# Kernel optimization log

Hardware: AMD Instinct MI355X
Metric: run time of the kernel (lower is better)

Reference implementation:

```python
import jax, jax.numpy as jnp
import numpy as np

MASK_GROUP = 8
RATIO = 0.125
K = max(1, min(MASK_GROUP, round(RATIO * MASK_GROUP)))  # = 1


def sparify_mask(outM):
    # top-k over the mask_group axis, scatter 1.0 at top-k positions
    _, idx = jax.lax.top_k(outM, K)              # [..., K]
    oh = jax.nn.one_hot(idx, outM.shape[-1], dtype=outM.dtype)  # [..., K, G]
    return jnp.sum(oh, axis=-2)                   # [..., G] 0/1 mask


def setup_inputs() -> dict:
    key = jax.random.key(0)
    ks = jax.random.split(key, 7)
    B, S, D, F = 4, 2048, 2048, 8192
    stdv = 1.0 / np.sqrt(F)
    u = lambda k, shape: jax.random.uniform(k, shape, jnp.float32, -stdv, stdv)
    return {
        "x": jax.random.normal(ks[0], (B, S, D), jnp.float32),
        "W1": u(ks[1], (F, D)),
        "b1": u(ks[2], (F,)),
        "Wm": u(ks[3], (MASK_GROUP, D)),
        "bm": u(ks[4], (MASK_GROUP,)),
        "W2": u(ks[5], (D, F)),
        "b2": u(ks[6], (D,)),
    }


def reference(x, W1, b1, Wm, bm, W2, b2):
    F_out = W1.shape[0]
    repeat_num = F_out // MASK_GROUP
    outL = jnp.einsum('bsd,fd->bsf', x, W1) + b1          # [B,S,F]
    outM = jax.nn.softmax(jnp.einsum('bsd,gd->bsg', x, Wm) + bm, axis=-1)  # [B,S,G]
    mask = sparify_mask(outM)                              # [B,S,G]
    gate = jnp.repeat(mask, repeat_num, axis=-1)           # [B,S,F]
    out2 = jax.nn.relu(outL * gate)
    out = jnp.einsum('bsf,df->bsd', out2, W2) + b2         # [B,S,D]
    return out
```

## Files before the change

### kernel.cpp

```cpp
#include <hip/hip_runtime.h>
#include <hip/hip_bf16.h>

#define T_TOK 8192
#define D_DIM 2048
#define F_DIM 8192
#define G_NUM 8
#define GF    1024

typedef __attribute__((ext_vector_type(8))) short bf16x8;
typedef __attribute__((ext_vector_type(4))) float f32x4;

__device__ __forceinline__ void async_load16(const void* g, void* l) {
    __builtin_amdgcn_global_load_lds(
        (const __attribute__((address_space(1))) unsigned int*)g,
        (__attribute__((address_space(3))) unsigned int*)l, 16, 0, 0);
}

__device__ __forceinline__ unsigned short f2bf(float f) {
    unsigned int u = __float_as_uint(f);
    unsigned int r = (u + 0x7fffu + ((u >> 16) & 1u)) >> 16;
    return (unsigned short)r;
}

__device__ __forceinline__ uint2 pack4(float4 v) {
    union { __hip_bfloat162 b; unsigned u; } c0, c1;
    c0.b = __float22bfloat162_rn({v.x, v.y});
    c1.b = __float22bfloat162_rn({v.z, v.w});
    uint2 r; r.x = c0.u; r.y = c1.u; return r;
}


__global__ void zero_cnt_kernel(int* __restrict__ cnt) {
    if (threadIdx.x < G_NUM) cnt[threadIdx.x] = 0;
}

__global__ __launch_bounds__(256)
void convert_kernel(const float* __restrict__ src, unsigned short* __restrict__ dst, int n) {
    int i = (blockIdx.x * 256 + threadIdx.x) * 8;
    if (i >= n) return;
    float4 a = *(const float4*)(src + i);
    float4 b = *(const float4*)(src + i + 4);
    uint2 p0 = pack4(a), p1 = pack4(b);
    uint4 o; o.x = p0.x; o.y = p0.y; o.z = p1.x; o.w = p1.y;
    *(uint4*)(dst + i) = o;
}

__global__ __launch_bounds__(256)
void gate_kernel(const float* __restrict__ x, const float* __restrict__ Wm,
                 const float* __restrict__ bm, int* __restrict__ cnt,
                 int* __restrict__ bucket) {
    const int wave  = threadIdx.x >> 6;
    const int lane  = threadIdx.x & 63;
    const int token = blockIdx.x * 4 + wave;
    const float* xr = x + (size_t)token * D_DIM;

    double acc[G_NUM];
#pragma unroll
    for (int g = 0; g < G_NUM; ++g) acc[g] = 0.0;

    for (int d = lane; d < D_DIM; d += 64) {
        float xv = xr[d];
#pragma unroll
        for (int g = 0; g < G_NUM; ++g)
            acc[g] += (double)xv * (double)Wm[g * D_DIM + d];
    }

#pragma unroll
    for (int g = 0; g < G_NUM; ++g) {
#pragma unroll
        for (int m = 32; m >= 1; m >>= 1)
            acc[g] += __shfl_xor(acc[g], m);
    }

    if (lane == 0) {
        double best = acc[0] + (double)bm[0];
        int bg = 0;
#pragma unroll
        for (int g = 1; g < G_NUM; ++g) {
            double v = acc[g] + (double)bm[g];
            if (v > best) { best = v; bg = g; }
        }
        int pos = atomicAdd(&cnt[bg], 1);
        bucket[bg * T_TOK + pos] = token;
    }
}

template <int KDIM, bool IS_G1, bool A_BF16, bool B_BF16>
__global__ __launch_bounds__(256)
void mfma_gemm(const void* __restrict__ Aop, const void* __restrict__ Bop,
               const float* __restrict__ bias,
               const int* __restrict__ cnt, const int* __restrict__ bucket,
               unsigned short* __restrict__ outH, float* __restrict__ outF) {
    const int g  = blockIdx.z;
    const int n  = cnt[g];
    const int t0 = blockIdx.y * 128;
    if (t0 >= n) return;
    const int nx0 = blockIdx.x * 128;
    const int tid  = threadIdx.x;
    const int lane = tid & 63;
    const int wv   = tid >> 6;

    __shared__ int toks[128];
    __shared__ __align__(16) unsigned short As[128 * 32];
    __shared__ __align__(16) unsigned short Bs[128 * 32];

    if (tid < 128) {
        int r = t0 + tid;
        if (r >= n) r = n - 1;
        toks[tid] = bucket[g * T_TOK + r];
    }
    __syncthreads();

    const size_t bstride = IS_G1 ? (size_t)KDIM : (size_t)F_DIM;
    const size_t brow0   = IS_G1 ? (size_t)(g * GF + nx0) : (size_t)nx0;
    const size_t bcol    = IS_G1 ? 0 : (size_t)(g * GF);

    const int lrow = tid >> 2;
    const int lseg = tid & 3;
    const unsigned short* aP0 = nullptr; const unsigned short* aP1 = nullptr;
    const unsigned short* bP0 = nullptr; const unsigned short* bP1 = nullptr;
    char *ldsA0 = nullptr, *ldsA1 = nullptr, *ldsB0 = nullptr, *ldsB1 = nullptr;
    if (A_BF16) {
        const unsigned short* Ab = (const unsigned short*)Aop;
        aP0 = Ab + (size_t)toks[lrow] * KDIM + lseg * 8;
        aP1 = Ab + (size_t)toks[64 + lrow] * KDIM + lseg * 8;
        ldsA0 = (char*)As + tid * 16;
        ldsA1 = (char*)As + 4096 + tid * 16;
    }
    if (B_BF16) {
        const unsigned short* Bb = (const unsigned short*)Bop;
        bP0 = Bb + (brow0 + lrow) * bstride + bcol + lseg * 8;
        bP1 = Bb + (brow0 + 64 + lrow) * bstride + bcol + lseg * 8;
        ldsB0 = (char*)Bs + tid * 16;
        ldsB1 = (char*)Bs + 4096 + tid * 16;
    }

    const int frw = tid >> 1;
    const int fsg = (tid & 1) * 16;
    const float* aF = nullptr; const float* bF = nullptr;
    char *ldsAf = nullptr, *ldsBf = nullptr;
    if (!A_BF16) {
        aF = (const float*)Aop + (size_t)toks[frw] * KDIM + fsg;
        ldsAf = (char*)As + frw * 64 + (tid & 1) * 32;
    }
    if (!B_BF16) {
        bF = (const float*)Bop + (brow0 + frw) * bstride + bcol + fsg;
        ldsBf = (char*)Bs + frw * 64 + (tid & 1) * 32;
    }

    f32x4 acc[4][4];
#pragma unroll
    for (int mi = 0; mi < 4; ++mi)
#pragma unroll
        for (int ni = 0; ni < 4; ++ni)
            acc[mi][ni] = (f32x4){0.f, 0.f, 0.f, 0.f};

    const int wr   = (wv >> 1) * 64;
    const int wc   = (wv & 1) * 64;
    const int frow = lane & 15;
    const int kh   = lane >> 4;

    for (int k0 = 0; k0 < KDIM; k0 += 32) {
        __syncthreads();
        if (A_BF16) { async_load16(aP0 + k0, ldsA0); async_load16(aP1 + k0, ldsA1); }
        if (B_BF16) { async_load16(bP0 + k0, ldsB0); async_load16(bP1 + k0, ldsB1); }
        if (!A_BF16) {
            float4 v0 = *(const float4*)(aF + k0);
            float4 v1 = *(const float4*)(aF + k0 + 4);
            float4 v2 = *(const float4*)(aF + k0 + 8);
            float4 v3 = *(const float4*)(aF + k0 + 12);
            uint2 p0 = pack4(v0), p1 = pack4(v1), p2 = pack4(v2), p3 = pack4(v3);
            uint4 w0; w0.x = p0.x; w0.y = p0.y; w0.z = p1.x; w0.w = p1.y;
            uint4 w1; w1.x = p2.x; w1.y = p2.y; w1.z = p3.x; w1.w = p3.y;
            *(uint4*)ldsAf = w0; *(uint4*)(ldsAf + 16) = w1;
        }
        if (!B_BF16) {
            float4 v0 = *(const float4*)(bF + k0);
            float4 v1 = *(const float4*)(bF + k0 + 4);
            float4 v2 = *(const float4*)(bF + k0 + 8);
            float4 v3 = *(const float4*)(bF + k0 + 12);
            uint2 p0 = pack4(v0), p1 = pack4(v1), p2 = pack4(v2), p3 = pack4(v3);
            uint4 w0; w0.x = p0.x; w0.y = p0.y; w0.z = p1.x; w0.w = p1.y;
            uint4 w1; w1.x = p2.x; w1.y = p2.y; w1.z = p3.x; w1.w = p3.y;
            *(uint4*)ldsBf = w0; *(uint4*)(ldsBf + 16) = w1;
        }
        __syncthreads();
        bf16x8 af[4], bfr[4];
#pragma unroll
        for (int mi = 0; mi < 4; ++mi)
            af[mi] = *(const bf16x8*)((const char*)As + (size_t)(wr + mi * 16 + frow) * 64 + kh * 16);
#pragma unroll
        for (int ni = 0; ni < 4; ++ni)
            bfr[ni] = *(const bf16x8*)((const char*)Bs + (size_t)(wc + ni * 16 + frow) * 64 + kh * 16);
#pragma unroll
        for (int mi = 0; mi < 4; ++mi)
#pragma unroll
            for (int ni = 0; ni < 4; ++ni)
                acc[mi][ni] = __builtin_amdgcn_mfma_f32_16x16x32_bf16(
                    af[mi], bfr[ni], acc[mi][ni], 0, 0, 0);
    }

    const float* bptr = bias + (IS_G1 ? (g * GF + nx0) : nx0);
    float bv[4];
#pragma unroll
    for (int ni = 0; ni < 4; ++ni) bv[ni] = bptr[wc + ni * 16 + frow];

#pragma unroll
    for (int mi = 0; mi < 4; ++mi) {
#pragma unroll
        for (int v = 0; v < 4; ++v) {
            int r = wr + mi * 16 + kh * 4 + v;
            if (t0 + r < n) {
                int tok = toks[r];
                if (IS_G1) {
                    unsigned short* dst = outH + (size_t)tok * GF + nx0 + wc + frow;
#pragma unroll
                    for (int ni = 0; ni < 4; ++ni) {
                        float o = fmaxf(acc[mi][ni][v] + bv[ni], 0.f);
                        dst[ni * 16] = f2bf(o);
                    }
                } else {
                    float* dst = outF + (size_t)tok * D_DIM + nx0 + wc + frow;
#pragma unroll
                    for (int ni = 0; ni < 4; ++ni)
                        dst[ni * 16] = acc[mi][ni][v] + bv[ni];
                }
            }
        }
    }
}

extern "C" void kernel_launch(void* const* d_in, const int* in_sizes, int n_in,
                              void* d_out, int out_size, void* d_ws, size_t ws_size,
                              hipStream_t stream) {
    const float* x  = (const float*)d_in[0];
    const float* W1 = (const float*)d_in[1];
    const float* b1 = (const float*)d_in[2];
    const float* Wm = (const float*)d_in[3];
    const float* bm = (const float*)d_in[4];
    const float* W2 = (const float*)d_in[5];
    const float* b2 = (const float*)d_in[6];
    float* out = (float*)d_out;

    int* cnt    = (int*)d_ws;
    int* bucket = (int*)((char*)d_ws + 1024);
    unsigned short* Hb  = (unsigned short*)((char*)d_ws + (1 << 19));
    unsigned short* xb  = Hb  + (size_t)T_TOK * GF;
    unsigned short* W1b = xb  + (size_t)T_TOK * D_DIM;
    unsigned short* W2b = W1b + (size_t)F_DIM * D_DIM;

    const bool fast = ws_size >= 117964800ull;
    const int NCVT = T_TOK * D_DIM;

    zero_cnt_kernel<<<1, 64, 0, stream>>>(cnt);
    gate_kernel<<<T_TOK / 4, 256, 0, stream>>>(x, Wm, bm, cnt, bucket);

    if (fast) {
        convert_kernel<<<NCVT / (256 * 8), 256, 0, stream>>>(x, xb, NCVT);
        convert_kernel<<<NCVT / (256 * 8), 256, 0, stream>>>(W1, W1b, NCVT);
        convert_kernel<<<NCVT / (256 * 8), 256, 0, stream>>>(W2, W2b, NCVT);
        mfma_gemm<D_DIM, true, true, true><<<dim3(GF / 128, T_TOK / 128, G_NUM), 256, 0, stream>>>(
            xb, W1b, b1, cnt, bucket, Hb, nullptr);
        mfma_gemm<GF, false, true, true><<<dim3(D_DIM / 128, T_TOK / 128, G_NUM), 256, 0, stream>>>(
            Hb, W2b, b2, cnt, bucket, nullptr, out);
    } else {
        mfma_gemm<D_DIM, true, false, false><<<dim3(GF / 128, T_TOK / 128, G_NUM), 256, 0, stream>>>(
            x, W1, b1, cnt, bucket, Hb, nullptr);
        mfma_gemm<GF, false, true, false><<<dim3(D_DIM / 128, T_TOK / 128, G_NUM), 256, 0, stream>>>(
            Hb, W2, b2, cnt, bucket, nullptr, out);
    }
}
```

Measured before the change: 468.2 us.

## Tile gate projection over token blocks and fuse x bf16 conversion into it

```diff
diff --git a/kernel.cpp b/kernel.cpp
--- a/kernel.cpp
+++ b/kernel.cpp
@@ -45,44 +45,99 @@
     *(uint4*)(dst + i) = o;
 }
 
+template <bool WRITE_XB>
+__global__ __launch_bounds__(64)
+void gate_partial_kernel(const float* __restrict__ x, const float* __restrict__ Wm,
+                         unsigned short* __restrict__ xb, double* __restrict__ part) {
+    const int q     = blockIdx.x;
+    const int t     = blockIdx.y;
+    const int lane  = threadIdx.x;
+    const int tok0  = t * 64;
+    const int kbase = q * 512;
+
+    __shared__ float wmS[8][512];
+    __shared__ float xs[64][68];
+
+    for (int i = lane * 4; i < 8 * 512; i += 64 * 4) {
+        int g = i >> 9, d = i & 511;
+        *(float4*)&wmS[g][d] = *(const float4*)(Wm + (size_t)g * D_DIM + kbase + d);
+    }
+
+    double acc[8] = {0, 0, 0, 0, 0, 0, 0, 0};
+
+    const int srow = lane >> 2;
+    const int scol = (lane & 3) * 4;
+
+    float4 v[16];
+#define LOAD_CHUNK(dbase_)                                                        \
+    _Pragma("unroll") for (int it = 0; it < 4; ++it)                              \
+    _Pragma("unroll") for (int ci = 0; ci < 4; ++ci) {                            \
+        int row = it * 16 + srow;                                                 \
+        int col = ci * 16 + scol;                                                 \
+        v[it * 4 + ci] = *(const float4*)(x + (size_t)(tok0 + row) * D_DIM +      \
+                                          kbase + (dbase_) + col);                \
+    }
+
+    LOAD_CHUNK(0)
+    __syncthreads();
+
+    for (int s = 0; s < 8; ++s) {
+        const int dbase = s * 64;
+#pragma unroll
+        for (int it = 0; it < 4; ++it)
+#pragma unroll
+            for (int ci = 0; ci < 4; ++ci) {
+                int row = it * 16 + srow;
+                int col = ci * 16 + scol;
+                *(float4*)&xs[row][col] = v[it * 4 + ci];
+                if (WRITE_XB) {
+                    uint2 p = pack4(v[it * 4 + ci]);
+                    *(uint2*)(xb + (size_t)(tok0 + row) * D_DIM + kbase + dbase + col) = p;
+                }
+            }
+        __syncthreads();
+        if (s < 7) { LOAD_CHUNK(dbase + 64) }
+#pragma unroll
+        for (int j4 = 0; j4 < 16; ++j4) {
+            float4 xv = *(const float4*)&xs[lane][j4 * 4];
+#pragma unroll
+            for (int g = 0; g < 8; ++g) {
+                float4 wv = *(const float4*)&wmS[g][dbase + j4 * 4];
+                acc[g] += (double)xv.x * (double)wv.x;
+                acc[g] += (double)xv.y * (double)wv.y;
+                acc[g] += (double)xv.z * (double)wv.z;
+                acc[g] += (double)xv.w * (double)wv.w;
+            }
+        }
+        __syncthreads();
+    }
+#undef LOAD_CHUNK
+
+    double* dst = part + (((size_t)t * 4 + q) * 64 + lane) * 8;
+#pragma unroll
+    for (int g = 0; g < 8; ++g) dst[g] = acc[g];
+}
+
 __global__ __launch_bounds__(256)
-void gate_kernel(const float* __restrict__ x, const float* __restrict__ Wm,
-                 const float* __restrict__ bm, int* __restrict__ cnt,
-                 int* __restrict__ bucket) {
-    const int wave  = threadIdx.x >> 6;
-    const int lane  = threadIdx.x & 63;
-    const int token = blockIdx.x * 4 + wave;
-    const float* xr = x + (size_t)token * D_DIM;
-
-    double acc[G_NUM];
-#pragma unroll
-    for (int g = 0; g < G_NUM; ++g) acc[g] = 0.0;
-
-    for (int d = lane; d < D_DIM; d += 64) {
-        float xv = xr[d];
-#pragma unroll
-        for (int g = 0; g < G_NUM; ++g)
-            acc[g] += (double)xv * (double)Wm[g * D_DIM + d];
-    }
-
-#pragma unroll
-    for (int g = 0; g < G_NUM; ++g) {
-#pragma unroll
-        for (int m = 32; m >= 1; m >>= 1)
-            acc[g] += __shfl_xor(acc[g], m);
-    }
-
-    if (lane == 0) {
-        double best = acc[0] + (double)bm[0];
-        int bg = 0;
-#pragma unroll
-        for (int g = 1; g < G_NUM; ++g) {
-            double v = acc[g] + (double)bm[g];
-            if (v > best) { best = v; bg = g; }
-        }
-        int pos = atomicAdd(&cnt[bg], 1);
-        bucket[bg * T_TOK + pos] = token;
-    }
+void gate_combine_kernel(const double* __restrict__ part, const float* __restrict__ bm,
+                         int* __restrict__ cnt, int* __restrict__ bucket) {
+    int tok = blockIdx.x * 256 + threadIdx.x;
+    int t = tok >> 6, L = tok & 63;
+    double s[8];
+#pragma unroll
+    for (int g = 0; g < 8; ++g) s[g] = (double)bm[g];
+#pragma unroll
+    for (int q = 0; q < 4; ++q) {
+        const double* p = part + (((size_t)t * 4 + q) * 64 + L) * 8;
+#pragma unroll
+        for (int g = 0; g < 8; ++g) s[g] += p[g];
+    }
+    double best = s[0]; int bg = 0;
+#pragma unroll
+    for (int g = 1; g < 8; ++g)
+        if (s[g] > best) { best = s[g]; bg = g; }
+    int pos = atomicAdd(&cnt[bg], 1);
+    bucket[bg * T_TOK + pos] = tok;
 }
 
 template <int KDIM, bool IS_G1, bool A_BF16, bool B_BF16>
@@ -244,25 +299,35 @@
 
     int* cnt    = (int*)d_ws;
     int* bucket = (int*)((char*)d_ws + 1024);
+    double* part = (double*)((char*)d_ws + (1 << 19));
     unsigned short* Hb  = (unsigned short*)((char*)d_ws + (1 << 19));
     unsigned short* xb  = Hb  + (size_t)T_TOK * GF;
     unsigned short* W1b = xb  + (size_t)T_TOK * D_DIM;
     unsigned short* W2b = W1b + (size_t)F_DIM * D_DIM;
 
     const bool fast = ws_size >= 117964800ull;
+    const bool mid  = ws_size >= 50855936ull;
     const int NCVT = T_TOK * D_DIM;
 
     zero_cnt_kernel<<<1, 64, 0, stream>>>(cnt);
-    gate_kernel<<<T_TOK / 4, 256, 0, stream>>>(x, Wm, bm, cnt, bucket);
+    if (fast || mid)
+        gate_partial_kernel<true><<<dim3(4, 128), 64, 0, stream>>>(x, Wm, xb, part);
+    else
+        gate_partial_kernel<false><<<dim3(4, 128), 64, 0, stream>>>(x, Wm, nullptr, part);
+    gate_combine_kernel<<<T_TOK / 256, 256, 0, stream>>>(part, bm, cnt, bucket);
 
     if (fast) {
-        convert_kernel<<<NCVT / (256 * 8), 256, 0, stream>>>(x, xb, NCVT);
         convert_kernel<<<NCVT / (256 * 8), 256, 0, stream>>>(W1, W1b, NCVT);
         convert_kernel<<<NCVT / (256 * 8), 256, 0, stream>>>(W2, W2b, NCVT);
         mfma_gemm<D_DIM, true, true, true><<<dim3(GF / 128, T_TOK / 128, G_NUM), 256, 0, stream>>>(
             xb, W1b, b1, cnt, bucket, Hb, nullptr);
         mfma_gemm<GF, false, true, true><<<dim3(D_DIM / 128, T_TOK / 128, G_NUM), 256, 0, stream>>>(
             Hb, W2b, b2, cnt, bucket, nullptr, out);
+    } else if (mid) {
+        mfma_gemm<D_DIM, true, true, false><<<dim3(GF / 128, T_TOK / 128, G_NUM), 256, 0, stream>>>(
+            xb, W1, b1, cnt, bucket, Hb, nullptr);
+        mfma_gemm<GF, false, true, false><<<dim3(D_DIM / 128, T_TOK / 128, G_NUM), 256, 0, stream>>>(
+            Hb, W2, b2, cnt, bucket, nullptr, out);
     } else {
         mfma_gemm<D_DIM, true, false, false><<<dim3(GF / 128, T_TOK / 128, G_NUM), 256, 0, stream>>>(
             x, W1, b1, cnt, bucket, Hb, nullptr);
```

New measurement: 406.2 us. 13.3% less time.
